# Optimization experiments

Measured on AMD Instinct MI355X. Metric: run time of the kernel, lower is better.

Reference implementation:

```python
import jax, jax.numpy as jnp
import numpy as np

EPS_DIST = 1e-8
EPS_BN = 1e-5


def _bn_relu(x, g, b):
    # training-mode BatchNorm1d over (batch, spatial) per channel, then ReLU
    mean = jnp.mean(x, axis=(0, 2), keepdims=True)
    var = jnp.mean((x - mean) ** 2, axis=(0, 2), keepdims=True)
    xhat = (x - mean) * jax.lax.rsqrt(var + EPS_BN)
    return jax.nn.relu(xhat * g[None, :, None] + b[None, :, None])


def setup_inputs() -> dict:
    key = jax.random.key(0)
    ks = jax.random.split(key, 8)
    B, N, M, C1, C2 = 8, 16384, 4096, 64, 256
    return {
        "p1": jax.random.normal(ks[0], (B, N, 3), jnp.float32),
        "p2": jax.random.normal(ks[1], (B, M, 3), jnp.float32),
        "f1": jax.random.normal(ks[2], (B, C1, N), jnp.float32),
        "f2": jax.random.normal(ks[3], (B, C2, M), jnp.float32),
        "idx": jax.random.randint(ks[4], (B, N, 3), 0, M, jnp.int64),
        "W1": jax.random.normal(ks[5], (256, C1 + C2), jnp.float32) * 0.05,
        "g1": jnp.ones((256,), jnp.float32),
        "b1": jnp.zeros((256,), jnp.float32),
        "W2": jax.random.normal(ks[6], (256, 256), jnp.float32) * 0.05,
        "g2": jnp.ones((256,), jnp.float32),
        "b2": jnp.zeros((256,), jnp.float32),
    }


def reference(p1, p2, f1, f2, idx, W1, g1, b1, W2, g2, b2):
    B = p1.shape[0]
    b_ix = jnp.arange(B)[:, None, None]  # batch index for gathers
    # --- three_interpolation: inverse-squared-distance weighted 3-NN interp ---
    nbr_xyz = p2[b_ix, idx]                     # [B, N, 3, 3]
    d2 = jnp.sum((p1[:, :, None, :] - nbr_xyz) ** 2, axis=-1)  # [B, N, 3]
    recip = 1.0 / (d2 + EPS_DIST)
    weight = recip / jnp.sum(recip, axis=-1, keepdims=True)    # [B, N, 3]
    f2_nbr = jnp.swapaxes(f2, 1, 2)[b_ix, idx]  # [B, N, 3, C2]
    interp = jnp.einsum("bnkc,bnk->bcn", f2_nbr, weight)       # [B, C2, N]
    # --- concat + two 1x1 conv + BN + ReLU blocks ---
    x = jnp.concatenate((f1, interp), axis=1)   # [B, C1+C2, N]
    x = _bn_relu(jnp.einsum("oi,bin->bon", W1, x), g1, b1)
    x = _bn_relu(jnp.einsum("oi,bin->bon", W2, x), g2, b2)
    return x
```

## Files before the change

### kernel.cpp

```cpp
#include <hip/hip_runtime.h>
#include <hip/hip_bf16.h>

#define BB 8
#define NN 16384
#define MM 4096
#define C1 64
#define C2 256
#define K1 320
#define CO 256
#define MTOT (BB * NN)

#define STATS_OFF 0
#define FLAG_OFF  8192
#define W1B_OFF   16384
#define W2B_OFF   180224
#define F2T_OFF   327680
#define XT_OFF    (327680 + 16777216)
#define H2_OFF    (327680 + 16777216 + 83886080)

typedef short v8s __attribute__((ext_vector_type(8)));
typedef float v4f __attribute__((ext_vector_type(4)));

__device__ __forceinline__ float bf2f(unsigned short u) {
    unsigned v = ((unsigned)u) << 16;
    float f;
    __builtin_memcpy(&f, &v, 4);
    return f;
}
__device__ __forceinline__ unsigned short f2bf(float f) {
    unsigned u;
    __builtin_memcpy(&u, &f, 4);
    unsigned r = u + 0x7fffu + ((u >> 16) & 1u);
    return (unsigned short)(r >> 16);
}
__device__ __forceinline__ void gload16(const unsigned short* g, unsigned short* l) {
    __builtin_amdgcn_global_load_lds((const __attribute__((address_space(1))) unsigned int*)g,
                                     (__attribute__((address_space(3))) unsigned int*)l, 16, 0, 0);
}

__global__ void k_prep(const void* idx_raw, int* flag64, float* stats,
                       const float* __restrict__ W1, unsigned short* __restrict__ W1b,
                       const float* __restrict__ W2, unsigned short* __restrict__ W2b) {
    int blk = blockIdx.x;
    int t = threadIdx.x;
    if (blk < 320) {
        int e = blk * 256 + t;
        W1b[e] = f2bf(W1[e]);
    } else if (blk < 576) {
        int e = (blk - 320) * 256 + t;
        W2b[e] = f2bf(W2[e]);
    } else {
        for (int i = t; i < 8 * 256; i += 256) stats[i] = 0.f;
        if (t == 0) {
            const int* a = (const int*)idx_raw;
            int all0 = 1;
            for (int j = 1; j < 64; j += 2) all0 &= (a[j] == 0);
            *flag64 = all0;
        }
    }
}

__global__ void k_tr_f2(const float* __restrict__ f2, unsigned short* __restrict__ f2t) {
    __shared__ float tile[64][33];
    int b = blockIdx.z;
    int c0 = blockIdx.y * 64;
    int m0 = blockIdx.x * 32;
    int t = threadIdx.x;
    int lm = t & 31, lc = t >> 5;
    const float* src = f2 + ((size_t)b * C2 + c0) * MM + m0;
#pragma unroll
    for (int j = 0; j < 8; ++j)
        tile[lc + 8 * j][lm] = src[(size_t)(lc + 8 * j) * MM + lm];
    __syncthreads();
    int m = t >> 3, c8 = (t & 7) * 8;
    unsigned short tmp[8];
#pragma unroll
    for (int k = 0; k < 8; ++k) tmp[k] = f2bf(tile[c8 + k][m]);
    uint4 v;
    v.x = (unsigned)tmp[0] | ((unsigned)tmp[1] << 16);
    v.y = (unsigned)tmp[2] | ((unsigned)tmp[3] << 16);
    v.z = (unsigned)tmp[4] | ((unsigned)tmp[5] << 16);
    v.w = (unsigned)tmp[6] | ((unsigned)tmp[7] << 16);
    *(uint4*)&f2t[((size_t)b * MM + m0 + m) * C2 + c0 + c8] = v;
}

__global__ void k_tr_f1(const float* __restrict__ f1, unsigned short* __restrict__ xT) {
    __shared__ float tile[64][33];
    int b = blockIdx.z;
    int n0 = blockIdx.x * 32;
    int t = threadIdx.x;
    int lm = t & 31, lc = t >> 5;
    const float* src = f1 + ((size_t)b * C1) * NN + n0;
#pragma unroll
    for (int j = 0; j < 8; ++j)
        tile[lc + 8 * j][lm] = src[(size_t)(lc + 8 * j) * NN + lm];
    __syncthreads();
    int m = t >> 3, c8 = (t & 7) * 8;
    unsigned short tmp[8];
#pragma unroll
    for (int k = 0; k < 8; ++k) tmp[k] = f2bf(tile[c8 + k][m]);
    uint4 v;
    v.x = (unsigned)tmp[0] | ((unsigned)tmp[1] << 16);
    v.y = (unsigned)tmp[2] | ((unsigned)tmp[3] << 16);
    v.z = (unsigned)tmp[4] | ((unsigned)tmp[5] << 16);
    v.w = (unsigned)tmp[6] | ((unsigned)tmp[7] << 16);
    *(uint4*)&xT[((size_t)b * NN + n0 + m) * K1 + c8] = v;
}

__global__ void k_interp(const float* __restrict__ p1, const float* __restrict__ p2,
                         const void* __restrict__ idxv, const int* __restrict__ flag64,
                         const unsigned short* __restrict__ f2t,
                         unsigned short* __restrict__ xT) {
    int t = threadIdx.x;
    int p = t >> 5, lane = t & 31;
    size_t pt = (size_t)blockIdx.x * 8 + p;
    int b = (int)(pt >> 14);
    int m0, m1, m2;
    if (*flag64) {
        const long long* id = (const long long*)idxv;
        m0 = (int)id[pt * 3 + 0]; m1 = (int)id[pt * 3 + 1]; m2 = (int)id[pt * 3 + 2];
    } else {
        const int* id = (const int*)idxv;
        m0 = id[pt * 3 + 0]; m1 = id[pt * 3 + 1]; m2 = id[pt * 3 + 2];
    }
    float qx = p1[pt * 3 + 0], qy = p1[pt * 3 + 1], qz = p1[pt * 3 + 2];
    const float* pb = p2 + (size_t)b * MM * 3;
    float dx, dy, dz;
    dx = qx - pb[m0 * 3 + 0]; dy = qy - pb[m0 * 3 + 1]; dz = qz - pb[m0 * 3 + 2];
    float d0 = dx * dx + dy * dy + dz * dz;
    dx = qx - pb[m1 * 3 + 0]; dy = qy - pb[m1 * 3 + 1]; dz = qz - pb[m1 * 3 + 2];
    float d1 = dx * dx + dy * dy + dz * dz;
    dx = qx - pb[m2 * 3 + 0]; dy = qy - pb[m2 * 3 + 1]; dz = qz - pb[m2 * 3 + 2];
    float d2v = dx * dx + dy * dy + dz * dz;
    float r0 = 1.f / (d0 + 1e-8f), r1 = 1.f / (d1 + 1e-8f), r2 = 1.f / (d2v + 1e-8f);
    float inv = 1.f / (r0 + r1 + r2);
    float w0 = r0 * inv, w1 = r1 * inv, w2 = r2 * inv;

    const unsigned short* fb = f2t + (size_t)b * MM * C2;
    int c0 = lane * 8;
    uint4 va = *(const uint4*)(fb + (size_t)m0 * C2 + c0);
    uint4 vb = *(const uint4*)(fb + (size_t)m1 * C2 + c0);
    uint4 vc = *(const uint4*)(fb + (size_t)m2 * C2 + c0);

    float r[8];
    {
        const unsigned av[4] = {va.x, va.y, va.z, va.w};
        const unsigned bv[4] = {vb.x, vb.y, vb.z, vb.w};
        const unsigned cv[4] = {vc.x, vc.y, vc.z, vc.w};
#pragma unroll
        for (int q = 0; q < 4; ++q) {
            r[2 * q + 0] = w0 * bf2f((unsigned short)(av[q] & 0xffff))
                         + w1 * bf2f((unsigned short)(bv[q] & 0xffff))
                         + w2 * bf2f((unsigned short)(cv[q] & 0xffff));
            r[2 * q + 1] = w0 * bf2f((unsigned short)(av[q] >> 16))
                         + w1 * bf2f((unsigned short)(bv[q] >> 16))
                         + w2 * bf2f((unsigned short)(cv[q] >> 16));
        }
    }
    uint4 outv;
    outv.x = (unsigned)f2bf(r[0]) | ((unsigned)f2bf(r[1]) << 16);
    outv.y = (unsigned)f2bf(r[2]) | ((unsigned)f2bf(r[3]) << 16);
    outv.z = (unsigned)f2bf(r[4]) | ((unsigned)f2bf(r[5]) << 16);
    outv.w = (unsigned)f2bf(r[6]) | ((unsigned)f2bf(r[7]) << 16);
    *(uint4*)(xT + pt * K1 + C1 + c0) = outv;
}

#define S_TK 64
__launch_bounds__(256)
__global__ void k_stats(const unsigned short* __restrict__ xT,
                        const unsigned short* __restrict__ W1b,
                        float* __restrict__ sum1, float* __restrict__ ssq1) {
    __shared__ unsigned short As[128 * S_TK];
    __shared__ unsigned short Bs[128 * S_TK];
    __shared__ float s_sum[128], s_ssq[128];
    const int t = threadIdx.x;
    const int lane = t & 63, w = t >> 6;
    const int wm = w >> 1, wc = w & 1;
    const long rbase = (long)blockIdx.x * 128;
    const int cb = blockIdx.y * 128;

    if (t < 128) { s_sum[t] = 0.f; s_ssq[t] = 0.f; }

    v4f acc[4][4];
#pragma unroll
    for (int r = 0; r < 4; ++r)
#pragma unroll
        for (int c = 0; c < 4; ++c) acc[r][c] = (v4f)(0.f);

    const int srow = w * 32 + (lane >> 3);
    const int sch = (lane & 7) * 8;
    const unsigned short* Ag = xT + (rbase + srow) * K1 + sch;
    const unsigned short* Bg = W1b + (size_t)(cb + srow) * K1 + sch;

    for (int k0 = 0; k0 < K1; k0 += S_TK) {
#pragma unroll
        for (int j = 0; j < 4; ++j) {
            gload16(Ag + (size_t)(j * 8) * K1 + k0, As + (w * 32 + j * 8) * S_TK);
            gload16(Bg + (size_t)(j * 8) * K1 + k0, Bs + (w * 32 + j * 8) * S_TK);
        }
        __syncthreads();
        const unsigned short* ApL = As + (wm * 64 + (lane & 15)) * S_TK + (lane >> 4) * 8;
        const unsigned short* BpL = Bs + (wc * 64 + (lane & 15)) * S_TK + (lane >> 4) * 8;
#pragma unroll
        for (int ks = 0; ks < 2; ++ks) {
            v8s af[4], bg[4];
#pragma unroll
            for (int r = 0; r < 4; ++r) af[r] = *(const v8s*)(ApL + r * 16 * S_TK + ks * 32);
#pragma unroll
            for (int c = 0; c < 4; ++c) bg[c] = *(const v8s*)(BpL + c * 16 * S_TK + ks * 32);
#pragma unroll
            for (int r = 0; r < 4; ++r)
#pragma unroll
                for (int c = 0; c < 4; ++c)
                    acc[r][c] = __builtin_amdgcn_mfma_f32_16x16x32_bf16(af[r], bg[c], acc[r][c], 0, 0, 0);
        }
        __syncthreads();
    }

    const int q = lane >> 4, ln = lane & 15;
#pragma unroll
    for (int c = 0; c < 4; ++c) {
        int col = wc * 64 + c * 16 + ln;
        float s = 0.f, sq = 0.f;
#pragma unroll
        for (int r = 0; r < 4; ++r)
#pragma unroll
            for (int i = 0; i < 4; ++i) {
                float v = acc[r][c][i];
                s += v; sq += v * v;
            }
        s += __shfl_xor(s, 16); s += __shfl_xor(s, 32);
        sq += __shfl_xor(sq, 16); sq += __shfl_xor(sq, 32);
        if (q == 0) {
            atomicAdd(&s_sum[col], s);
            atomicAdd(&s_ssq[col], sq);
        }
    }
    __syncthreads();
    if (t < 128) {
        atomicAdd(&sum1[cb + t], s_sum[t]);
        atomicAdd(&ssq1[cb + t], s_ssq[t]);
    }
}

__launch_bounds__(256)
__global__ void k_fused(const unsigned short* __restrict__ xT,
                        const unsigned short* __restrict__ W1b,
                        const unsigned short* __restrict__ W2b,
                        const float* __restrict__ sum1, const float* __restrict__ ssq1,
                        const float* __restrict__ g1, const float* __restrict__ b1,
                        unsigned short* __restrict__ h2,
                        float* __restrict__ sum2, float* __restrict__ ssq2) {
    __shared__ unsigned short smAB[64 * 64 + 256 * 64];
    __shared__ unsigned short Ys[64 * 256];
    __shared__ float sc1[CO], sh1[CO], s_sum[CO], s_ssq[CO];
    unsigned short* As = smAB;
    unsigned short* Bs = smAB + 64 * 64;

    const int t = threadIdx.x;
    const int lane = t & 63, w = t >> 6;
    const int q = lane >> 4, ln = lane & 15;
    const long rbm = (long)blockIdx.x * 64;

    {
        const float invn = 1.f / (float)MTOT;
        float m = sum1[t] * invn;
        float v = ssq1[t] * invn - m * m;
        float s = g1[t] * rsqrtf(v + 1e-5f);
        sc1[t] = s;
        sh1[t] = b1[t] - m * s;
        s_sum[t] = 0.f; s_ssq[t] = 0.f;
    }
    __syncthreads();

    v4f acc[4][4];
#pragma unroll
    for (int r = 0; r < 4; ++r)
#pragma unroll
        for (int c = 0; c < 4; ++c) acc[r][c] = (v4f)(0.f);

    const int sr8 = lane >> 3, sc8 = (lane & 7) * 8;

    for (int k0 = 0; k0 < K1; k0 += 64) {
#pragma unroll
        for (int j = 0; j < 2; ++j)
            gload16(xT + (size_t)(rbm + w * 16 + j * 8 + sr8) * K1 + k0 + sc8,
                    As + (w * 16 + j * 8) * 64);
#pragma unroll
        for (int j = 0; j < 8; ++j)
            gload16(W1b + (size_t)(w * 64 + j * 8 + sr8) * K1 + k0 + sc8,
                    Bs + (w * 64 + j * 8) * 64);
        __syncthreads();
        const unsigned short* ApL = As + ln * 64 + q * 8;
        const unsigned short* BpL = Bs + (w * 64 + ln) * 64 + q * 8;
#pragma unroll
        for (int ks = 0; ks < 2; ++ks) {
            v8s af[4], bg[4];
#pragma unroll
            for (int r = 0; r < 4; ++r) af[r] = *(const v8s*)(ApL + r * 16 * 64 + ks * 32);
#pragma unroll
            for (int c = 0; c < 4; ++c) bg[c] = *(const v8s*)(BpL + c * 16 * 64 + ks * 32);
#pragma unroll
            for (int r = 0; r < 4; ++r)
#pragma unroll
                for (int c = 0; c < 4; ++c)
                    acc[r][c] = __builtin_amdgcn_mfma_f32_16x16x32_bf16(af[r], bg[c], acc[r][c], 0, 0, 0);
        }
        __syncthreads();
    }

#pragma unroll
    for (int c = 0; c < 4; ++c) {
        int col = w * 64 + c * 16 + ln;
        float sv = sc1[col], hv = sh1[col];
        int kc = col >> 3, ci = col & 7;
#pragma unroll
        for (int r = 0; r < 4; ++r)
#pragma unroll
            for (int i = 0; i < 4; ++i) {
                int row = r * 16 + q * 4 + i;
                float y = fmaxf(acc[r][c][i] * sv + hv, 0.f);
                Ys[row * 256 + 8 * (kc ^ (row & 15)) + ci] = f2bf(y);
            }
    }
    __syncthreads();

#pragma unroll
    for (int r = 0; r < 4; ++r)
#pragma unroll
        for (int c = 0; c < 4; ++c) acc[r][c] = (v4f)(0.f);

    for (int k0 = 0; k0 < CO; k0 += 64) {
#pragma unroll
        for (int j = 0; j < 8; ++j)
            gload16(W2b + (size_t)(w * 64 + j * 8 + sr8) * CO + k0 + sc8,
                    Bs + (w * 64 + j * 8) * 64);
        __syncthreads();
        const unsigned short* BpL = Bs + (w * 64 + ln) * 64 + q * 8;
#pragma unroll
        for (int ks = 0; ks < 2; ++ks) {
            v8s af[4], bg[4];
            int kc2 = (k0 >> 3) + ks * 4 + q;
#pragma unroll
            for (int r = 0; r < 4; ++r)
                af[r] = *(const v8s*)&Ys[(r * 16 + ln) * 256 + 8 * (kc2 ^ ln)];
#pragma unroll
            for (int c = 0; c < 4; ++c) bg[c] = *(const v8s*)(BpL + c * 16 * 64 + ks * 32);
#pragma unroll
            for (int r = 0; r < 4; ++r)
#pragma unroll
                for (int c = 0; c < 4; ++c)
                    acc[r][c] = __builtin_amdgcn_mfma_f32_16x16x32_bf16(af[r], bg[c], acc[r][c], 0, 0, 0);
        }
        __syncthreads();
    }

#pragma unroll
    for (int c = 0; c < 4; ++c) {
        int col = w * 64 + c * 16 + ln;
        int cc = col >> 3, ci = col & 7;
        float s = 0.f, sq = 0.f;
#pragma unroll
        for (int r = 0; r < 4; ++r)
#pragma unroll
            for (int i = 0; i < 4; ++i) {
                int row = r * 16 + q * 4 + i;
                float v = acc[r][c][i];
                smAB[row * 256 + 8 * (cc ^ (row & 15)) + ci] = f2bf(v);
                s += v; sq += v * v;
            }
        s += __shfl_xor(s, 16); s += __shfl_xor(s, 32);
        sq += __shfl_xor(sq, 16); sq += __shfl_xor(sq, 32);
        if (q == 0) {
            atomicAdd(&s_sum[col], s);
            atomicAdd(&s_ssq[col], sq);
        }
    }
    __syncthreads();
    {
        int row2 = t >> 5, cc2 = t & 31;
#pragma unroll
        for (int j = 0; j < 8; ++j) {
            int row = row2 + 8 * j;
            uint4 v = *(const uint4*)&smAB[row * 256 + 8 * (cc2 ^ (row & 15))];
            *(uint4*)&h2[(size_t)(rbm + row) * CO + cc2 * 8] = v;
        }
    }
    atomicAdd(&sum2[t], s_sum[t]);
    atomicAdd(&ssq2[t], s_ssq[t]);
}

__global__ void k_apply(const unsigned short* __restrict__ h2,
                        const float* __restrict__ sum2, const float* __restrict__ ssq2,
                        const float* __restrict__ g2, const float* __restrict__ b2,
                        float* __restrict__ out) {
    __shared__ float T[64][36];
    __shared__ float sc[64], sh[64];
    int b = blockIdx.z;
    int cb = blockIdx.y * 64;
    int n0 = blockIdx.x * 32;
    int t = threadIdx.x;
    if (t < 64) {
        const float invn = 1.f / (float)MTOT;
        int o = cb + t;
        float m = sum2[o] * invn;
        float v = ssq2[o] * invn - m * m;
        float s = g2[o] * rsqrtf(v + 1e-5f);
        sc[t] = s;
        sh[t] = b2[o] - m * s;
    }
    __syncthreads();
    {
        int nl = t >> 3, oc = (t & 7) * 8;
        uint4 hv = *(const uint4*)&h2[((size_t)b * NN + n0 + nl) * CO + cb + oc];
        const unsigned uv[4] = {hv.x, hv.y, hv.z, hv.w};
#pragma unroll
        for (int k = 0; k < 4; ++k) {
            int ch0 = oc + 2 * k;
            T[ch0 + 0][nl] = fmaxf(bf2f((unsigned short)(uv[k] & 0xffff)) * sc[ch0] + sh[ch0], 0.f);
            T[ch0 + 1][nl] = fmaxf(bf2f((unsigned short)(uv[k] >> 16)) * sc[ch0 + 1] + sh[ch0 + 1], 0.f);
        }
    }
    __syncthreads();
    {
        int o = t >> 2, jb = t & 3;
#pragma unroll
        for (int j2 = 0; j2 < 2; ++j2) {
            int j = jb + j2 * 4;
            float4 v = *(const float4*)&T[o][j * 4];
            *(float4*)&out[((size_t)(b * CO + cb + o)) * NN + n0 + j * 4] = v;
        }
    }
}

extern "C" void kernel_launch(void* const* d_in, const int* in_sizes, int n_in,
                              void* d_out, int out_size, void* d_ws, size_t ws_size,
                              hipStream_t stream) {
    const float* p1 = (const float*)d_in[0];
    const float* p2 = (const float*)d_in[1];
    const float* f1 = (const float*)d_in[2];
    const float* f2 = (const float*)d_in[3];
    const void*  idx = d_in[4];
    const float* W1 = (const float*)d_in[5];
    const float* g1 = (const float*)d_in[6];
    const float* b1 = (const float*)d_in[7];
    const float* W2 = (const float*)d_in[8];
    const float* g2 = (const float*)d_in[9];
    const float* b2 = (const float*)d_in[10];
    float* out = (float*)d_out;

    char* ws = (char*)d_ws;
    float* stats = (float*)(ws + STATS_OFF);
    float* sum1 = stats + 0;     float* ssq1 = stats + 256;
    float* sum2 = stats + 1024;  float* ssq2 = stats + 1280;
    int* flag64 = (int*)(ws + FLAG_OFF);
    unsigned short* W1b = (unsigned short*)(ws + W1B_OFF);
    unsigned short* W2b = (unsigned short*)(ws + W2B_OFF);
    unsigned short* f2t = (unsigned short*)(ws + F2T_OFF);
    unsigned short* xT  = (unsigned short*)(ws + XT_OFF);
    unsigned short* h2  = (unsigned short*)(ws + H2_OFF);

    k_prep<<<577, 256, 0, stream>>>(idx, flag64, stats, W1, W1b, W2, W2b);
    k_tr_f2<<<dim3(MM / 32, C2 / 64, BB), 256, 0, stream>>>(f2, f2t);
    k_tr_f1<<<dim3(NN / 32, 1, BB), 256, 0, stream>>>(f1, xT);
    k_interp<<<MTOT / 8, 256, 0, stream>>>(p1, p2, idx, flag64, f2t, xT);
    k_stats<<<dim3(MTOT / 128, 2), 256, 0, stream>>>(xT, W1b, sum1, ssq1);
    k_fused<<<MTOT / 64, 256, 0, stream>>>(xT, W1b, W2b, sum1, ssq1, g1, b1, h2, sum2, ssq2);
    k_apply<<<dim3(NN / 32, CO / 64, BB), 256, 0, stream>>>(h2, sum2, ssq2, g2, b2, out);
}
```

Before: 427.0 us.

## Split fused MLP into separate GEMMs with materialized bf16 intermediate

Replaces the stats-recompute GEMM plus fused two-GEMM kernel with a single templated GEMM kernel run twice, plus an elementwise BN+ReLU pass over a bf16 intermediate stored in the output buffer. This removes the duplicated first-layer GEMM and LDS staging, loading MFMA fragments directly from global memory. In exchange it adds a full round trip of the intermediate activations through memory and uses scattered 2-byte stores.

```diff
diff --git a/kernel.cpp b/kernel.cpp
--- a/kernel.cpp
+++ b/kernel.cpp
@@ -32,10 +32,6 @@
     __builtin_memcpy(&u, &f, 4);
     unsigned r = u + 0x7fffu + ((u >> 16) & 1u);
     return (unsigned short)(r >> 16);
-}
-__device__ __forceinline__ void gload16(const unsigned short* g, unsigned short* l) {
-    __builtin_amdgcn_global_load_lds((const __attribute__((address_space(1))) unsigned int*)g,
-                                     (__attribute__((address_space(3))) unsigned int*)l, 16, 0, 0);
 }
 
 __global__ void k_prep(const void* idx_raw, int* flag64, float* stats,
@@ -165,21 +161,21 @@
     *(uint4*)(xT + pt * K1 + C1 + c0) = outv;
 }
 
-#define S_TK 64
+template <int KDIM>
 __launch_bounds__(256)
-__global__ void k_stats(const unsigned short* __restrict__ xT,
-                        const unsigned short* __restrict__ W1b,
-                        float* __restrict__ sum1, float* __restrict__ ssq1) {
-    __shared__ unsigned short As[128 * S_TK];
-    __shared__ unsigned short Bs[128 * S_TK];
-    __shared__ float s_sum[128], s_ssq[128];
+__global__ void k_gemm_bf(const unsigned short* __restrict__ A,
+                          const unsigned short* __restrict__ W,
+                          unsigned short* __restrict__ O,
+                          float* __restrict__ sum, float* __restrict__ ssq) {
+    __shared__ float s_sum[64], s_ssq[64];
     const int t = threadIdx.x;
     const int lane = t & 63, w = t >> 6;
-    const int wm = w >> 1, wc = w & 1;
-    const long rbase = (long)blockIdx.x * 128;
-    const int cb = blockIdx.y * 128;
-
-    if (t < 128) { s_sum[t] = 0.f; s_ssq[t] = 0.f; }
+    const int q = lane >> 4, ln = lane & 15;
+    const long rb = (long)blockIdx.x * 256 + w * 64;
+    const int cb = blockIdx.y * 64;
+
+    if (t < 64) { s_sum[t] = 0.f; s_ssq[t] = 0.f; }
+    __syncthreads();
 
     v4f acc[4][4];
 #pragma unroll
@@ -187,207 +183,83 @@
 #pragma unroll
         for (int c = 0; c < 4; ++c) acc[r][c] = (v4f)(0.f);
 
-    const int srow = w * 32 + (lane >> 3);
-    const int sch = (lane & 7) * 8;
-    const unsigned short* Ag = xT + (rbase + srow) * K1 + sch;
-    const unsigned short* Bg = W1b + (size_t)(cb + srow) * K1 + sch;
-
-    for (int k0 = 0; k0 < K1; k0 += S_TK) {
-#pragma unroll
-        for (int j = 0; j < 4; ++j) {
-            gload16(Ag + (size_t)(j * 8) * K1 + k0, As + (w * 32 + j * 8) * S_TK);
-            gload16(Bg + (size_t)(j * 8) * K1 + k0, Bs + (w * 32 + j * 8) * S_TK);
-        }
-        __syncthreads();
-        const unsigned short* ApL = As + (wm * 64 + (lane & 15)) * S_TK + (lane >> 4) * 8;
-        const unsigned short* BpL = Bs + (wc * 64 + (lane & 15)) * S_TK + (lane >> 4) * 8;
-#pragma unroll
-        for (int ks = 0; ks < 2; ++ks) {
-            v8s af[4], bg[4];
-#pragma unroll
-            for (int r = 0; r < 4; ++r) af[r] = *(const v8s*)(ApL + r * 16 * S_TK + ks * 32);
-#pragma unroll
-            for (int c = 0; c < 4; ++c) bg[c] = *(const v8s*)(BpL + c * 16 * S_TK + ks * 32);
-#pragma unroll
-            for (int r = 0; r < 4; ++r)
-#pragma unroll
-                for (int c = 0; c < 4; ++c)
-                    acc[r][c] = __builtin_amdgcn_mfma_f32_16x16x32_bf16(af[r], bg[c], acc[r][c], 0, 0, 0);
-        }
-        __syncthreads();
-    }
-
-    const int q = lane >> 4, ln = lane & 15;
+    const unsigned short* Ab = A + (size_t)(rb + ln) * KDIM + q * 8;
+    const unsigned short* Bb = W + (size_t)(cb + ln) * KDIM + q * 8;
+
+#pragma unroll
+    for (int ks = 0; ks < KDIM / 32; ++ks) {
+        v8s af[4], bf[4];
+#pragma unroll
+        for (int r = 0; r < 4; ++r)
+            af[r] = *(const v8s*)(Ab + (size_t)(r * 16) * KDIM + ks * 32);
+#pragma unroll
+        for (int c = 0; c < 4; ++c)
+            bf[c] = *(const v8s*)(Bb + (size_t)(c * 16) * KDIM + ks * 32);
+#pragma unroll
+        for (int r = 0; r < 4; ++r)
+#pragma unroll
+            for (int c = 0; c < 4; ++c)
+                acc[r][c] = __builtin_amdgcn_mfma_f32_16x16x32_bf16(af[r], bf[c], acc[r][c], 0, 0, 0);
+    }
+
 #pragma unroll
     for (int c = 0; c < 4; ++c) {
-        int col = wc * 64 + c * 16 + ln;
         float s = 0.f, sq = 0.f;
 #pragma unroll
         for (int r = 0; r < 4; ++r)
 #pragma unroll
             for (int i = 0; i < 4; ++i) {
                 float v = acc[r][c][i];
+                O[(size_t)(rb + r * 16 + q * 4 + i) * CO + cb + c * 16 + ln] = f2bf(v);
                 s += v; sq += v * v;
             }
         s += __shfl_xor(s, 16); s += __shfl_xor(s, 32);
         sq += __shfl_xor(sq, 16); sq += __shfl_xor(sq, 32);
         if (q == 0) {
-            atomicAdd(&s_sum[col], s);
-            atomicAdd(&s_ssq[col], sq);
-        }
-    }
-    __syncthreads();
-    if (t < 128) {
-        atomicAdd(&sum1[cb + t], s_sum[t]);
-        atomicAdd(&ssq1[cb + t], s_ssq[t]);
-    }
-}
-
-__launch_bounds__(256)
-__global__ void k_fused(const unsigned short* __restrict__ xT,
-                        const unsigned short* __restrict__ W1b,
-                        const unsigned short* __restrict__ W2b,
-                        const float* __restrict__ sum1, const float* __restrict__ ssq1,
-                        const float* __restrict__ g1, const float* __restrict__ b1,
-                        unsigned short* __restrict__ h2,
-                        float* __restrict__ sum2, float* __restrict__ ssq2) {
-    __shared__ unsigned short smAB[64 * 64 + 256 * 64];
-    __shared__ unsigned short Ys[64 * 256];
-    __shared__ float sc1[CO], sh1[CO], s_sum[CO], s_ssq[CO];
-    unsigned short* As = smAB;
-    unsigned short* Bs = smAB + 64 * 64;
-
-    const int t = threadIdx.x;
-    const int lane = t & 63, w = t >> 6;
-    const int q = lane >> 4, ln = lane & 15;
-    const long rbm = (long)blockIdx.x * 64;
-
+            atomicAdd(&s_sum[c * 16 + ln], s);
+            atomicAdd(&s_ssq[c * 16 + ln], sq);
+        }
+    }
+    __syncthreads();
+    if (t < 64) {
+        atomicAdd(&sum[cb + t], s_sum[t]);
+        atomicAdd(&ssq[cb + t], s_ssq[t]);
+    }
+}
+
+__global__ void k_y(unsigned short* __restrict__ h1,
+                    const float* __restrict__ sum1, const float* __restrict__ ssq1,
+                    const float* __restrict__ g1, const float* __restrict__ b1) {
+    __shared__ float sc[256], sh[256];
+    int t = threadIdx.x;
     {
         const float invn = 1.f / (float)MTOT;
         float m = sum1[t] * invn;
         float v = ssq1[t] * invn - m * m;
         float s = g1[t] * rsqrtf(v + 1e-5f);
-        sc1[t] = s;
-        sh1[t] = b1[t] - m * s;
-        s_sum[t] = 0.f; s_ssq[t] = 0.f;
-    }
-    __syncthreads();
-
-    v4f acc[4][4];
-#pragma unroll
-    for (int r = 0; r < 4; ++r)
-#pragma unroll
-        for (int c = 0; c < 4; ++c) acc[r][c] = (v4f)(0.f);
-
-    const int sr8 = lane >> 3, sc8 = (lane & 7) * 8;
-
-    for (int k0 = 0; k0 < K1; k0 += 64) {
-#pragma unroll
-        for (int j = 0; j < 2; ++j)
-            gload16(xT + (size_t)(rbm + w * 16 + j * 8 + sr8) * K1 + k0 + sc8,
-                    As + (w * 16 + j * 8) * 64);
-#pragma unroll
-        for (int j = 0; j < 8; ++j)
-            gload16(W1b + (size_t)(w * 64 + j * 8 + sr8) * K1 + k0 + sc8,
-                    Bs + (w * 64 + j * 8) * 64);
-        __syncthreads();
-        const unsigned short* ApL = As + ln * 64 + q * 8;
-        const unsigned short* BpL = Bs + (w * 64 + ln) * 64 + q * 8;
-#pragma unroll
-        for (int ks = 0; ks < 2; ++ks) {
-            v8s af[4], bg[4];
-#pragma unroll
-            for (int r = 0; r < 4; ++r) af[r] = *(const v8s*)(ApL + r * 16 * 64 + ks * 32);
-#pragma unroll
-            for (int c = 0; c < 4; ++c) bg[c] = *(const v8s*)(BpL + c * 16 * 64 + ks * 32);
-#pragma unroll
-            for (int r = 0; r < 4; ++r)
-#pragma unroll
-                for (int c = 0; c < 4; ++c)
-                    acc[r][c] = __builtin_amdgcn_mfma_f32_16x16x32_bf16(af[r], bg[c], acc[r][c], 0, 0, 0);
-        }
-        __syncthreads();
-    }
-
-#pragma unroll
-    for (int c = 0; c < 4; ++c) {
-        int col = w * 64 + c * 16 + ln;
-        float sv = sc1[col], hv = sh1[col];
-        int kc = col >> 3, ci = col & 7;
-#pragma unroll
-        for (int r = 0; r < 4; ++r)
-#pragma unroll
-            for (int i = 0; i < 4; ++i) {
-                int row = r * 16 + q * 4 + i;
-                float y = fmaxf(acc[r][c][i] * sv + hv, 0.f);
-                Ys[row * 256 + 8 * (kc ^ (row & 15)) + ci] = f2bf(y);
-            }
-    }
-    __syncthreads();
-
-#pragma unroll
-    for (int r = 0; r < 4; ++r)
-#pragma unroll
-        for (int c = 0; c < 4; ++c) acc[r][c] = (v4f)(0.f);
-
-    for (int k0 = 0; k0 < CO; k0 += 64) {
-#pragma unroll
-        for (int j = 0; j < 8; ++j)
-            gload16(W2b + (size_t)(w * 64 + j * 8 + sr8) * CO + k0 + sc8,
-                    Bs + (w * 64 + j * 8) * 64);
-        __syncthreads();
-        const unsigned short* BpL = Bs + (w * 64 + ln) * 64 + q * 8;
-#pragma unroll
-        for (int ks = 0; ks < 2; ++ks) {
-            v8s af[4], bg[4];
-            int kc2 = (k0 >> 3) + ks * 4 + q;
-#pragma unroll
-            for (int r = 0; r < 4; ++r)
-                af[r] = *(const v8s*)&Ys[(r * 16 + ln) * 256 + 8 * (kc2 ^ ln)];
-#pragma unroll
-            for (int c = 0; c < 4; ++c) bg[c] = *(const v8s*)(BpL + c * 16 * 64 + ks * 32);
-#pragma unroll
-            for (int r = 0; r < 4; ++r)
-#pragma unroll
-                for (int c = 0; c < 4; ++c)
-                    acc[r][c] = __builtin_amdgcn_mfma_f32_16x16x32_bf16(af[r], bg[c], acc[r][c], 0, 0, 0);
-        }
-        __syncthreads();
-    }
-
-#pragma unroll
-    for (int c = 0; c < 4; ++c) {
-        int col = w * 64 + c * 16 + ln;
-        int cc = col >> 3, ci = col & 7;
-        float s = 0.f, sq = 0.f;
-#pragma unroll
-        for (int r = 0; r < 4; ++r)
-#pragma unroll
-            for (int i = 0; i < 4; ++i) {
-                int row = r * 16 + q * 4 + i;
-                float v = acc[r][c][i];
-                smAB[row * 256 + 8 * (cc ^ (row & 15)) + ci] = f2bf(v);
-                s += v; sq += v * v;
-            }
-        s += __shfl_xor(s, 16); s += __shfl_xor(s, 32);
-        sq += __shfl_xor(sq, 16); sq += __shfl_xor(sq, 32);
-        if (q == 0) {
-            atomicAdd(&s_sum[col], s);
-            atomicAdd(&s_ssq[col], sq);
-        }
-    }
-    __syncthreads();
-    {
-        int row2 = t >> 5, cc2 = t & 31;
-#pragma unroll
-        for (int j = 0; j < 8; ++j) {
-            int row = row2 + 8 * j;
-            uint4 v = *(const uint4*)&smAB[row * 256 + 8 * (cc2 ^ (row & 15))];
-            *(uint4*)&h2[(size_t)(rbm + row) * CO + cc2 * 8] = v;
-        }
-    }
-    atomicAdd(&sum2[t], s_sum[t]);
-    atomicAdd(&ssq2[t], s_ssq[t]);
+        sc[t] = s;
+        sh[t] = b1[t] - m * s;
+    }
+    __syncthreads();
+    size_t i = ((size_t)blockIdx.x * 256 + t) * 8;
+    int ch = (int)(i & 255);
+    uint4 hv = *(const uint4*)(h1 + i);
+    const unsigned uv[4] = {hv.x, hv.y, hv.z, hv.w};
+    unsigned short o[8];
+#pragma unroll
+    for (int k = 0; k < 4; ++k) {
+        int c0 = ch + 2 * k;
+        float lo = fmaxf(bf2f((unsigned short)(uv[k] & 0xffff)) * sc[c0] + sh[c0], 0.f);
+        float hi = fmaxf(bf2f((unsigned short)(uv[k] >> 16)) * sc[c0 + 1] + sh[c0 + 1], 0.f);
+        o[2 * k] = f2bf(lo);
+        o[2 * k + 1] = f2bf(hi);
+    }
+    uint4 ov;
+    ov.x = (unsigned)o[0] | ((unsigned)o[1] << 16);
+    ov.y = (unsigned)o[2] | ((unsigned)o[3] << 16);
+    ov.z = (unsigned)o[4] | ((unsigned)o[5] << 16);
+    ov.w = (unsigned)o[6] | ((unsigned)o[7] << 16);
+    *(uint4*)(h1 + i) = ov;
 }
 
 __global__ void k_apply(const unsigned short* __restrict__ h2,
@@ -460,11 +332,14 @@
     unsigned short* xT  = (unsigned short*)(ws + XT_OFF);
     unsigned short* h2  = (unsigned short*)(ws + H2_OFF);
 
+    unsigned short* h1 = (unsigned short*)d_out;
+
     k_prep<<<577, 256, 0, stream>>>(idx, flag64, stats, W1, W1b, W2, W2b);
     k_tr_f2<<<dim3(MM / 32, C2 / 64, BB), 256, 0, stream>>>(f2, f2t);
     k_tr_f1<<<dim3(NN / 32, 1, BB), 256, 0, stream>>>(f1, xT);
     k_interp<<<MTOT / 8, 256, 0, stream>>>(p1, p2, idx, flag64, f2t, xT);
-    k_stats<<<dim3(MTOT / 128, 2), 256, 0, stream>>>(xT, W1b, sum1, ssq1);
-    k_fused<<<MTOT / 64, 256, 0, stream>>>(xT, W1b, W2b, sum1, ssq1, g1, b1, h2, sum2, ssq2);
+    k_gemm_bf<K1><<<dim3(MTOT / 256, CO / 64), 256, 0, stream>>>(xT, W1b, h1, sum1, ssq1);
+    k_y<<<MTOT * CO / 8 / 256, 256, 0, stream>>>(h1, sum1, ssq1, g1, b1);
+    k_gemm_bf<CO><<<dim3(MTOT / 256, CO / 64), 256, 0, stream>>>(h1, W2b, h2, sum2, ssq2);
     k_apply<<<dim3(NN / 32, CO / 64, BB), 256, 0, stream>>>(h2, sum2, ssq2, g2, b2, out);
 }
```

Result: slower. 488.8 us (+14.5%).
